# Performance work log

Measured on AMD Instinct MI355X. Metric: run time of the kernel, lower is better.

The kernel has to match this reference:

```python
import jax, jax.numpy as jnp
import numpy as np
import math

B, S, E = 4, 2048, 1024


def setup_inputs() -> dict:
    key = jax.random.key(0)
    ks = jax.random.split(key, 7)
    w_scale = 1.0 / math.sqrt(E)
    x = jax.random.normal(ks[0], (B, S, E), dtype=jnp.float32)
    Wq = jax.random.normal(ks[1], (E, E), dtype=jnp.float32) * w_scale
    bq = jax.random.normal(ks[2], (E,), dtype=jnp.float32) * 0.01
    Wk = jax.random.normal(ks[3], (E, E), dtype=jnp.float32) * w_scale
    bk = jax.random.normal(ks[4], (E,), dtype=jnp.float32) * 0.01
    Wv = jax.random.normal(ks[5], (E, E), dtype=jnp.float32) * w_scale
    bv = jax.random.normal(ks[6], (E,), dtype=jnp.float32) * 0.01
    # causal mask: True = attend, False = masked (mask == 0 -> -inf)
    mask = jnp.broadcast_to(jnp.tril(jnp.ones((S, S), dtype=bool)), (B, S, S))
    return {"x": x, "Wq": Wq, "bq": bq, "Wk": Wk, "bk": bk, "Wv": Wv, "bv": bv, "mask": mask}


def reference(x, Wq, bq, Wk, bk, Wv, bv, mask):
    # nn.Linear stores weight as [out, in]: y = x @ W.T + b
    Q = jnp.einsum("bse,oe->bso", x, Wq) + bq
    K = jnp.einsum("bse,oe->bso", x, Wk) + bk
    V = jnp.einsum("bse,oe->bso", x, Wv) + bv
    scale = math.sqrt(E)
    scores = jnp.einsum("bqe,bke->bqk", Q, K) / scale  # [B,S,S]
    scores = jnp.where(mask, scores, -jnp.inf)
    attn = jax.nn.softmax(scores, axis=-1)
    out = jnp.einsum("bqk,bke->bqe", attn, V)  # [B,S,E]
    return out
```

## Files before the change

kernel.cpp:

```cpp
#include <hip/hip_runtime.h>
#include <stdint.h>

typedef unsigned short u16;
typedef __attribute__((ext_vector_type(8))) short bf16x8;
typedef __attribute__((ext_vector_type(4))) float f32x4;

#define MFMA16(a, b, c) __builtin_amdgcn_mfma_f32_16x16x32_bf16((a), (b), (c), 0, 0, 0)

#define MASKVAL (-1.0e30f)

__device__ __forceinline__ u16 f2bf(float f) {
  union { float f; uint32_t u; } v; v.f = f;
  uint32_t u = v.u;
  u += 0x7fffu + ((u >> 16) & 1u);
  return (u16)(u >> 16);
}
__device__ __forceinline__ void async16(const void* g, void* l) {
  __builtin_amdgcn_global_load_lds(
      (const __attribute__((address_space(1))) unsigned int*)g,
      (__attribute__((address_space(3))) unsigned int*)l, 16, 0, 0);
}

__global__ __launch_bounds__(256) void conv_kernel(
    const float* __restrict__ x,  const float* __restrict__ wq,
    const float* __restrict__ wk, const float* __restrict__ wv,
    u16* __restrict__ xb, u16* __restrict__ wb, int do_wv)
{
  const int NX = 1 << 20;
  const int NW = 1 << 17;
  const int total = NX + NW * (do_wv ? 3 : 2);
  for (int i = blockIdx.x * 256 + threadIdx.x; i < total; i += gridDim.x * 256) {
    const float* src; u16* dst;
    if (i < NX) {
      src = x + (size_t)i * 8;
      const int m = i >> 7, k8 = i & 127;
      dst = xb + (size_t)m * 2048 + 1024 + k8 * 8;
    } else {
      const int j = i - NX;
      const int wsel = j >> 17;
      const int jj = j & (NW - 1);
      const float* W = (wsel == 0) ? wq : (wsel == 1) ? wk : wv;
      const int zoff = (wsel == 0) ? 0 : (wsel == 1) ? (2 << 20) : (1 << 20);
      src = W + (size_t)jj * 8;
      dst = wb + zoff + jj * 8;
    }
    float4 f0 = *(const float4*)src;
    float4 f1 = *(const float4*)(src + 4);
    ushort4 h0, h1;
    h0.x = f2bf(f0.x); h0.y = f2bf(f0.y); h0.z = f2bf(f0.z); h0.w = f2bf(f0.w);
    h1.x = f2bf(f1.x); h1.y = f2bf(f1.y); h1.z = f2bf(f1.z); h1.w = f2bf(f1.w);
    *(ushort4*)dst = h0;
    *(ushort4*)(dst + 4) = h1;
  }
}

template <int BMODE>
__global__ __launch_bounds__(256) void gemm_kernel(
    const u16* __restrict__ xb,
    const u16* __restrict__ wb,
    const float* __restrict__ wv_f,
    const float* __restrict__ bq, const float* __restrict__ bk,
    const float* __restrict__ bv,
    u16* __restrict__ q_out, u16* __restrict__ vt_out, u16* __restrict__ k_out,
    int zbase, int zmul)
{
  const int z = zbase + (int)blockIdx.z * zmul;
  __shared__ u16 lA[2][128 * 32];
  __shared__ u16 lB[2][128 * 32];

  const int m0 = blockIdx.x * 128, n0 = blockIdx.y * 128;
  const int tid = threadIdx.x, lane = tid & 63, w = tid >> 6;
  const int quad = lane >> 4, l15 = lane & 15;
  const int wr = (w >> 1) * 64, wc = (w & 1) * 64;

  const u16* wz = wb + ((size_t)z << 20);
  const float* bias = (z == 0) ? bq : (z == 1) ? bv : bk;

  const int sr  = lane >> 2;
  const int ssw = (lane >> 3) & 3;
  const int c16s = (lane & 3) ^ ssw;

  auto stageA = [&](int kk, int bbuf) {
    const int k0 = kk * 32;
#pragma unroll
    for (int i = 0; i < 2; ++i) {
      const int r = w * 32 + i * 16 + sr;
      async16(&xb[(size_t)(m0 + r) * 2048 + 1024 + k0 + c16s * 8],
              &lA[bbuf][w * 1024 + i * 512]);
    }
  };
  auto stageB = [&](int kk, int bbuf) {
    const int k0 = kk * 32;
#pragma unroll
    for (int i = 0; i < 2; ++i) {
      const int r = w * 32 + i * 16 + sr;
      async16(&wz[(size_t)(n0 + r) * 1024 + k0 + c16s * 8],
              &lB[bbuf][w * 1024 + i * 512]);
    }
  };

  float4 bfr[4];
  const int br = tid >> 1;
  const int bcb = (tid & 1) * 2;
  const int bs = (br >> 1) & 3;
  auto loadB = [&](int kk) {
    const float* p = &wv_f[(size_t)(n0 + br) * 1024 + kk * 32 + bcb * 8];
    bfr[0] = ((const float4*)p)[0];
    bfr[1] = ((const float4*)p)[1];
    bfr[2] = ((const float4*)p)[2];
    bfr[3] = ((const float4*)p)[3];
  };
  auto writeB = [&](int bbuf) {
    ushort4 h[4];
#pragma unroll
    for (int g = 0; g < 4; ++g) {
      h[g].x = f2bf(bfr[g].x); h[g].y = f2bf(bfr[g].y);
      h[g].z = f2bf(bfr[g].z); h[g].w = f2bf(bfr[g].w);
    }
    const int p0 = (bcb + 0) ^ bs, p1 = (bcb + 1) ^ bs;
    *(ushort4*)&lB[bbuf][br * 32 + p0 * 8]     = h[0];
    *(ushort4*)&lB[bbuf][br * 32 + p0 * 8 + 4] = h[1];
    *(ushort4*)&lB[bbuf][br * 32 + p1 * 8]     = h[2];
    *(ushort4*)&lB[bbuf][br * 32 + p1 * 8 + 4] = h[3];
  };

  f32x4 zero4 = {0.f, 0.f, 0.f, 0.f};
  f32x4 acc[4][4];
#pragma unroll
  for (int i = 0; i < 4; ++i)
#pragma unroll
    for (int j = 0; j < 4; ++j) acc[i][j] = zero4;

  if constexpr (BMODE == 0) {
    stageA(0, 0); stageB(0, 0);
  } else {
    stageA(0, 0); loadB(0); writeB(0);
  }

  const int fxor = (l15 >> 1) & 3;
  for (int kk = 0; kk < 32; ++kk) {
    const int bbuf = kk & 1;
    __syncthreads();
    if (kk + 1 < 32) {
      stageA(kk + 1, bbuf ^ 1);
      if constexpr (BMODE == 0) stageB(kk + 1, bbuf ^ 1);
      else loadB(kk + 1);
    }
    bf16x8 af[4], bw[4];
#pragma unroll
    for (int mf = 0; mf < 4; ++mf)
      af[mf] = *(const bf16x8*)
          &lA[bbuf][(wr + mf * 16 + l15) * 32 + (quad ^ fxor) * 8];
#pragma unroll
    for (int nf = 0; nf < 4; ++nf)
      bw[nf] = *(const bf16x8*)
          &lB[bbuf][(wc + nf * 16 + l15) * 32 + (quad ^ fxor) * 8];
#pragma unroll
    for (int mf = 0; mf < 4; ++mf)
#pragma unroll
      for (int nf = 0; nf < 4; ++nf)
        acc[mf][nf] = MFMA16(af[mf], bw[nf], acc[mf][nf]);
    if constexpr (BMODE == 1) {
      if (kk + 1 < 32) writeB(bbuf ^ 1);
    }
  }

  float bvv[4];
#pragma unroll
  for (int nf = 0; nf < 4; ++nf)
    bvv[nf] = bias[n0 + wc + nf * 16 + l15];

  if (z == 0) {
    const float qs = 0.03125f;
#pragma unroll
    for (int mf = 0; mf < 4; ++mf) {
#pragma unroll
      for (int nf = 0; nf < 4; ++nf) {
        const int n = n0 + wc + nf * 16 + l15;
#pragma unroll
        for (int r = 0; r < 4; ++r) {
          const int m = m0 + wr + mf * 16 + quad * 4 + r;
          q_out[(size_t)m * 2048 + n] = f2bf((acc[mf][nf][r] + bvv[nf]) * qs);
        }
      }
    }
  } else if (z == 1) {
#pragma unroll
    for (int mf = 0; mf < 4; ++mf) {
      const int mbase = m0 + wr + mf * 16 + quad * 4;
      const int bb = mbase >> 11;
      const int ss = mbase & 2047;
#pragma unroll
      for (int nf = 0; nf < 4; ++nf) {
        const int n = n0 + wc + nf * 16 + l15;
        ushort4 pk;
        pk.x = f2bf(acc[mf][nf][0] + bvv[nf]);
        pk.y = f2bf(acc[mf][nf][1] + bvv[nf]);
        pk.z = f2bf(acc[mf][nf][2] + bvv[nf]);
        pk.w = f2bf(acc[mf][nf][3] + bvv[nf]);
        *(ushort4*)&vt_out[((size_t)bb << 21) + (size_t)n * 2048 + ss] = pk;
      }
    }
  } else {
#pragma unroll
    for (int mf = 0; mf < 4; ++mf) {
#pragma unroll
      for (int nf = 0; nf < 4; ++nf) {
        const int n = n0 + wc + nf * 16 + l15;
#pragma unroll
        for (int r = 0; r < 4; ++r) {
          const int m = m0 + wr + mf * 16 + quad * 4 + r;
          k_out[(size_t)m * 1024 + n] = f2bf(acc[mf][nf][r] + bvv[nf]);
        }
      }
    }
  }
}

__global__ __launch_bounds__(256) void attn_kernel(
    const u16* Q, const u16* __restrict__ K,
    const u16* __restrict__ VT, float* out)
{
  __shared__ u16   sQ[32 * 1024];
  __shared__ u16   sKV[2][128 * 128];
  __shared__ float sS[32 * 132];
  __shared__ u16   sP[32 * 136];
  __shared__ float sAlpha[32];
  __shared__ float sLinv[32];

  const int lin = blockIdx.x + ((int)blockIdx.y << 6);
  const int xcd = lin & 7;
  const int t = ((lin >> 3) << 1) | (xcd & 1);
  const int b = xcd >> 1;
  const int q0 = t * 32;
  const int tid = threadIdx.x, lane = tid & 63, w = tid >> 6;
  const int quad = lane >> 4, l15 = lane & 15;
  const u16* Qb  = Q  + ((size_t)b << 22);
  const u16* Kb  = K  + ((size_t)b << 21);
  const u16* VTb = VT + ((size_t)b << 21);
  float* outb = out + ((size_t)b << 21);

  const int sr = lane >> 4;
  const int sp = lane & 15;

#pragma unroll
  for (int jj = 0; jj < 16; ++jj) {
    const int j = w * 16 + jj;
    const int r = j >> 1;
    const int p = (j & 1) * 64 + lane;
    const int cq = p ^ (r & 15);
    async16(&Qb[(size_t)(q0 + r) * 2048 + (size_t)cq * 8], &sQ[j * 512]);
  }

  auto issueK = [&](int kv0, int e0, u16* buf) {
#pragma unroll
    for (int jj = 0; jj < 8; ++jj) {
      const int j = w * 8 + jj;
      const int r = j * 4 + sr;
      const int c16 = sp ^ (r & 15);
      async16(&Kb[(size_t)(kv0 + r) * 1024 + e0 + c16 * 8], buf + j * 512);
    }
  };
  auto issueV = [&](int kv0, int ck, u16* buf) {
#pragma unroll
    for (int jj = 0; jj < 8; ++jj) {
      const int j = w * 8 + jj;
      const int r = j * 4 + sr;
      const int c16 = sp ^ (r & 15);
      async16(&VTb[(size_t)(ck * 128 + r) * 2048 + kv0 + c16 * 8], buf + j * 512);
    }
  };

  f32x4 zero4 = {0.f, 0.f, 0.f, 0.f};
  f32x4 accO[8][2][2];
#pragma unroll
  for (int c = 0; c < 8; ++c)
#pragma unroll
    for (int i = 0; i < 2; ++i)
#pragma unroll
      for (int j = 0; j < 2; ++j) accO[c][i][j] = zero4;

  float m_i = MASKVAL, l_i = 0.f;
  const int srow = tid >> 3, slane = tid & 7;

  issueK(0, 0, sKV[0]);

  const int niter = q0 / 128 + 1;
  for (int it = 0; it < niter; ++it) {
    const int kv0 = it * 128;

    f32x4 accS[2][2];
#pragma unroll
    for (int i = 0; i < 2; ++i)
#pragma unroll
      for (int j = 0; j < 2; ++j) accS[i][j] = zero4;

#pragma unroll
    for (int c = 0; c < 8; ++c) {
      __syncthreads();
      if (c < 7) issueK(kv0, (c + 1) * 128, sKV[(c + 1) & 1]);
      else       issueV(kv0, 0, sKV[0]);
      const u16* buf = sKV[c & 1];
#pragma unroll
      for (int ks = 0; ks < 4; ++ks) {
        const int cq = c * 16 + ks * 4 + quad;
        const int ck = ks * 4 + quad;
        bf16x8 a0 = *(const bf16x8*)&sQ[l15 * 1024 + (cq ^ l15) * 8];
        bf16x8 a1 = *(const bf16x8*)&sQ[(16 + l15) * 1024 + (cq ^ l15) * 8];
        bf16x8 b0 = *(const bf16x8*)&buf[(w * 32 + l15) * 128 + (ck ^ l15) * 8];
        bf16x8 b1 = *(const bf16x8*)&buf[(w * 32 + 16 + l15) * 128 + (ck ^ l15) * 8];
        accS[0][0] = MFMA16(a0, b0, accS[0][0]);
        accS[0][1] = MFMA16(a0, b1, accS[0][1]);
        accS[1][0] = MFMA16(a1, b0, accS[1][0]);
        accS[1][1] = MFMA16(a1, b1, accS[1][1]);
      }
    }

#pragma unroll
    for (int mf = 0; mf < 2; ++mf)
#pragma unroll
      for (int nf = 0; nf < 2; ++nf)
#pragma unroll
        for (int r = 0; r < 4; ++r) {
          const int row = mf * 16 + quad * 4 + r;
          const int col = w * 32 + nf * 16 + l15;
          sS[row * 132 + col] =
              (kv0 + col <= q0 + row) ? accS[mf][nf][r] : MASKVAL;
        }
    __syncthreads();

    {
      float v[16];
      float4 t0 = *(const float4*)&sS[srow * 132 + slane * 16 + 0];
      float4 t1 = *(const float4*)&sS[srow * 132 + slane * 16 + 4];
      float4 t2 = *(const float4*)&sS[srow * 132 + slane * 16 + 8];
      float4 t3 = *(const float4*)&sS[srow * 132 + slane * 16 + 12];
      v[0]=t0.x; v[1]=t0.y; v[2]=t0.z; v[3]=t0.w;
      v[4]=t1.x; v[5]=t1.y; v[6]=t1.z; v[7]=t1.w;
      v[8]=t2.x; v[9]=t2.y; v[10]=t2.z; v[11]=t2.w;
      v[12]=t3.x; v[13]=t3.y; v[14]=t3.z; v[15]=t3.w;
      float mx = v[0];
#pragma unroll
      for (int j = 1; j < 16; ++j) mx = fmaxf(mx, v[j]);
#pragma unroll
      for (int d = 1; d < 8; d <<= 1) mx = fmaxf(mx, __shfl_xor(mx, d, 64));
      const float mnew  = fmaxf(m_i, mx);
      const float alpha = __expf(m_i - mnew);
      float sum = 0.f;
      u16 pb[16];
#pragma unroll
      for (int j = 0; j < 16; ++j) {
        const float p = __expf(v[j] - mnew);
        pb[j] = f2bf(p);
        union { uint32_t u; float f; } pv; pv.u = ((uint32_t)pb[j]) << 16;
        sum += pv.f;
      }
#pragma unroll
      for (int g = 0; g < 4; ++g) {
        ushort4 pk; pk.x = pb[g*4]; pk.y = pb[g*4+1]; pk.z = pb[g*4+2]; pk.w = pb[g*4+3];
        *(ushort4*)&sP[srow * 136 + slane * 16 + g * 4] = pk;
      }
#pragma unroll
      for (int d = 1; d < 8; d <<= 1) sum += __shfl_xor(sum, d, 64);
      l_i = l_i * alpha + sum;
      m_i = mnew;
      if (slane == 0) sAlpha[srow] = alpha;
      if (it == niter - 1 && slane == 0) sLinv[srow] = 1.0f / l_i;
    }
    __syncthreads();

    float av[2][4];
#pragma unroll
    for (int mf = 0; mf < 2; ++mf)
#pragma unroll
      for (int r = 0; r < 4; ++r)
        av[mf][r] = sAlpha[mf * 16 + quad * 4 + r];
#pragma unroll
    for (int c = 0; c < 8; ++c)
#pragma unroll
      for (int mf = 0; mf < 2; ++mf)
#pragma unroll
        for (int nf = 0; nf < 2; ++nf)
#pragma unroll
          for (int r = 0; r < 4; ++r) accO[c][mf][nf][r] *= av[mf][r];

#pragma unroll
    for (int k = 0; k < 8; ++k) {
      if (k > 0) __syncthreads();
      if (k < 7) issueV(kv0, k + 1, sKV[(k + 1) & 1]);
      else if (it + 1 < niter) issueK(kv0 + 128, 0, sKV[0]);
      const u16* buf = sKV[k & 1];
#pragma unroll
      for (int ks = 0; ks < 4; ++ks) {
        const int ck = ks * 4 + quad;
        bf16x8 p0 = *(const bf16x8*)&sP[l15 * 136 + ks * 32 + quad * 8];
        bf16x8 p1 = *(const bf16x8*)&sP[(16 + l15) * 136 + ks * 32 + quad * 8];
        bf16x8 v0 = *(const bf16x8*)&buf[(w * 32 + l15) * 128 + (ck ^ l15) * 8];
        bf16x8 v1 = *(const bf16x8*)&buf[(w * 32 + 16 + l15) * 128 + (ck ^ l15) * 8];
        accO[k][0][0] = MFMA16(p0, v0, accO[k][0][0]);
        accO[k][0][1] = MFMA16(p0, v1, accO[k][0][1]);
        accO[k][1][0] = MFMA16(p1, v0, accO[k][1][0]);
        accO[k][1][1] = MFMA16(p1, v1, accO[k][1][1]);
      }
    }
  }

  float lv[2][4];
#pragma unroll
  for (int mf = 0; mf < 2; ++mf)
#pragma unroll
    for (int r = 0; r < 4; ++r)
      lv[mf][r] = sLinv[mf * 16 + quad * 4 + r];
#pragma unroll
  for (int c = 0; c < 8; ++c)
#pragma unroll
    for (int mf = 0; mf < 2; ++mf)
#pragma unroll
      for (int nf = 0; nf < 2; ++nf) {
        const int col = c * 128 + w * 32 + nf * 16 + l15;
#pragma unroll
        for (int r = 0; r < 4; ++r) {
          const int row = q0 + mf * 16 + quad * 4 + r;
          outb[(size_t)row * 1024 + col] = accO[c][mf][nf][r] * lv[mf][r];
        }
      }
}

extern "C" void kernel_launch(void* const* d_in, const int* in_sizes, int n_in,
                              void* d_out, int out_size, void* d_ws, size_t ws_size,
                              hipStream_t stream) {
  (void)in_sizes; (void)n_in; (void)out_size;
  const float* x  = (const float*)d_in[0];
  const float* Wq = (const float*)d_in[1];
  const float* bq = (const float*)d_in[2];
  const float* Wk = (const float*)d_in[3];
  const float* bk = (const float*)d_in[4];
  const float* Wv = (const float*)d_in[5];
  const float* bv = (const float*)d_in[6];

  u16* qbuf = (u16*)d_out;
  u16* vtw  = (u16*)d_in[7];
  u16* kw   = (u16*)d_ws;

  const bool ws_big = ws_size >= (size_t)22 * 1024 * 1024;
  u16* wb = ws_big ? (u16*)d_ws + (8u << 20) : (u16*)d_in[7];

  conv_kernel<<<dim3(2048), 256, 0, stream>>>(x, Wq, Wk, Wv, qbuf, wb,
                                              ws_big ? 1 : 0);
  if (ws_big) {
    gemm_kernel<0><<<dim3(64, 8, 3), 256, 0, stream>>>(
        qbuf, wb, Wv, bq, bk, bv, qbuf, vtw, kw, 0, 1);
  } else {
    gemm_kernel<0><<<dim3(64, 8, 2), 256, 0, stream>>>(
        qbuf, wb, Wv, bq, bk, bv, qbuf, vtw, kw, 0, 2);
    gemm_kernel<1><<<dim3(64, 8, 1), 256, 0, stream>>>(
        qbuf, wb, Wv, bq, bk, bv, qbuf, vtw, kw, 1, 1);
  }

  attn_kernel<<<dim3(64, 4), 256, 0, stream>>>(qbuf, kw, vtw, (float*)d_out);
}
```

Measured before the change: 435.0 us.

## Restructure attention kernel to 512 threads with triple-buffered K/V/Q ring

The attention kernel now runs 8 waves per block instead of 4, each wave owning 16 key/value columns, and the whole-Q shared tile is replaced by streaming Q chunks alongside K chunks. A three-slot ring buffer with explicit vmcnt waits and raw barriers replaces double buffering with __syncthreads, so loads are issued two stages ahead. This is meant to raise latency hiding and reduce LDS footprint and per-thread accumulator registers. It adds redundant Q reloads every kv iteration and depends on hand-tuned waitcnt values being correct.

New measurement: 414.4 us. -4.7%, faster.

```diff
diff --git a/kernel.cpp b/kernel.cpp
--- a/kernel.cpp
+++ b/kernel.cpp
@@ -8,6 +8,10 @@
 #define MFMA16(a, b, c) __builtin_amdgcn_mfma_f32_16x16x32_bf16((a), (b), (c), 0, 0, 0)
 
 #define MASKVAL (-1.0e30f)
+
+#define WAITV(N) asm volatile("s_waitcnt vmcnt(" #N ")" ::: "memory")
+#define LGKM0()  asm volatile("s_waitcnt lgkmcnt(0)" ::: "memory")
+#define SBAR()   __builtin_amdgcn_s_barrier()
 
 __device__ __forceinline__ u16 f2bf(float f) {
   union { float f; uint32_t u; } v; v.f = f;
@@ -217,12 +221,12 @@
   }
 }
 
-__global__ __launch_bounds__(256) void attn_kernel(
-    const u16* Q, const u16* __restrict__ K,
+__global__ __launch_bounds__(512) void attn_kernel(
+    const u16* __restrict__ Q, const u16* __restrict__ K,
     const u16* __restrict__ VT, float* out)
 {
-  __shared__ u16   sQ[32 * 1024];
-  __shared__ u16   sKV[2][128 * 128];
+  constexpr int SLOT = 20480;
+  __shared__ u16   ring[3][SLOT];
   __shared__ float sS[32 * 132];
   __shared__ u16   sP[32 * 136];
   __shared__ float sAlpha[32];
@@ -243,131 +247,122 @@
   const int sr = lane >> 4;
   const int sp = lane & 15;
 
-#pragma unroll
-  for (int jj = 0; jj < 16; ++jj) {
-    const int j = w * 16 + jj;
-    const int r = j >> 1;
-    const int p = (j & 1) * 64 + lane;
-    const int cq = p ^ (r & 15);
-    async16(&Qb[(size_t)(q0 + r) * 2048 + (size_t)cq * 8], &sQ[j * 512]);
-  }
-
-  auto issueK = [&](int kv0, int e0, u16* buf) {
-#pragma unroll
-    for (int jj = 0; jj < 8; ++jj) {
-      const int j = w * 8 + jj;
+  auto issueK = [&](int kv0, int e0, u16* slot) {
+#pragma unroll
+    for (int jj = 0; jj < 4; ++jj) {
+      const int j = w * 4 + jj;
       const int r = j * 4 + sr;
       const int c16 = sp ^ (r & 15);
-      async16(&Kb[(size_t)(kv0 + r) * 1024 + e0 + c16 * 8], buf + j * 512);
-    }
-  };
-  auto issueV = [&](int kv0, int ck, u16* buf) {
-#pragma unroll
-    for (int jj = 0; jj < 8; ++jj) {
-      const int j = w * 8 + jj;
+      async16(&Kb[(size_t)(kv0 + r) * 1024 + e0 + c16 * 8], slot + j * 512);
+    }
+  };
+  auto issueV = [&](int kv0, int ck, u16* slot) {
+#pragma unroll
+    for (int jj = 0; jj < 4; ++jj) {
+      const int j = w * 4 + jj;
       const int r = j * 4 + sr;
       const int c16 = sp ^ (r & 15);
-      async16(&VTb[(size_t)(ck * 128 + r) * 2048 + kv0 + c16 * 8], buf + j * 512);
-    }
+      async16(&VTb[(size_t)(ck * 128 + r) * 2048 + kv0 + c16 * 8], slot + j * 512);
+    }
+  };
+  auto issueQ = [&](int cq, u16* slot) {
+    const int r = w * 4 + sr;
+    const int c16 = sp ^ (r & 15);
+    async16(&Qb[(size_t)(q0 + r) * 2048 + cq * 128 + c16 * 8],
+            slot + 16384 + w * 512);
   };
 
   f32x4 zero4 = {0.f, 0.f, 0.f, 0.f};
-  f32x4 accO[8][2][2];
+  f32x4 accO[8][2];
 #pragma unroll
   for (int c = 0; c < 8; ++c)
 #pragma unroll
-    for (int i = 0; i < 2; ++i)
-#pragma unroll
-      for (int j = 0; j < 2; ++j) accO[c][i][j] = zero4;
+    for (int i = 0; i < 2; ++i) accO[c][i] = zero4;
 
   float m_i = MASKVAL, l_i = 0.f;
-  const int srow = tid >> 3, slane = tid & 7;
-
-  issueK(0, 0, sKV[0]);
+  const int srow = tid >> 4, slane = tid & 15;
+
+  issueK(0, 0, ring[0]);   issueQ(0, ring[0]);
+  issueK(0, 128, ring[1]); issueQ(1, ring[1]);
+  int sl = 0, sl2 = 2;
 
   const int niter = q0 / 128 + 1;
   for (int it = 0; it < niter; ++it) {
     const int kv0 = it * 128;
 
-    f32x4 accS[2][2];
-#pragma unroll
-    for (int i = 0; i < 2; ++i)
-#pragma unroll
-      for (int j = 0; j < 2; ++j) accS[i][j] = zero4;
+    f32x4 accS[2];
+    accS[0] = zero4; accS[1] = zero4;
 
 #pragma unroll
     for (int c = 0; c < 8; ++c) {
-      __syncthreads();
-      if (c < 7) issueK(kv0, (c + 1) * 128, sKV[(c + 1) & 1]);
-      else       issueV(kv0, 0, sKV[0]);
-      const u16* buf = sKV[c & 1];
+      if (c < 7) { WAITV(5); } else { WAITV(4); }
+      SBAR();
+      u16* dst = ring[sl2];
+      if (c < 6)      { issueK(kv0, (c + 2) * 128, dst); issueQ(c + 2, dst); }
+      else if (c == 6) issueV(kv0, 0, dst);
+      else             issueV(kv0, 1, dst);
+      const u16* bufK = ring[sl];
+      const u16* bufQ = ring[sl] + 16384;
 #pragma unroll
       for (int ks = 0; ks < 4; ++ks) {
-        const int cq = c * 16 + ks * 4 + quad;
-        const int ck = ks * 4 + quad;
-        bf16x8 a0 = *(const bf16x8*)&sQ[l15 * 1024 + (cq ^ l15) * 8];
-        bf16x8 a1 = *(const bf16x8*)&sQ[(16 + l15) * 1024 + (cq ^ l15) * 8];
-        bf16x8 b0 = *(const bf16x8*)&buf[(w * 32 + l15) * 128 + (ck ^ l15) * 8];
-        bf16x8 b1 = *(const bf16x8*)&buf[(w * 32 + 16 + l15) * 128 + (ck ^ l15) * 8];
-        accS[0][0] = MFMA16(a0, b0, accS[0][0]);
-        accS[0][1] = MFMA16(a0, b1, accS[0][1]);
-        accS[1][0] = MFMA16(a1, b0, accS[1][0]);
-        accS[1][1] = MFMA16(a1, b1, accS[1][1]);
-      }
+        const int cc = ks * 4 + quad;
+        bf16x8 a0 = *(const bf16x8*)&bufQ[l15 * 128 + (cc ^ l15) * 8];
+        bf16x8 a1 = *(const bf16x8*)&bufQ[(16 + l15) * 128 + (cc ^ l15) * 8];
+        bf16x8 b0 = *(const bf16x8*)&bufK[(w * 16 + l15) * 128 + (cc ^ l15) * 8];
+        accS[0] = MFMA16(a0, b0, accS[0]);
+        accS[1] = MFMA16(a1, b0, accS[1]);
+      }
+      sl  = (sl  == 2) ? 0 : sl  + 1;
+      sl2 = (sl2 == 2) ? 0 : sl2 + 1;
     }
 
 #pragma unroll
     for (int mf = 0; mf < 2; ++mf)
 #pragma unroll
-      for (int nf = 0; nf < 2; ++nf)
-#pragma unroll
-        for (int r = 0; r < 4; ++r) {
-          const int row = mf * 16 + quad * 4 + r;
-          const int col = w * 32 + nf * 16 + l15;
-          sS[row * 132 + col] =
-              (kv0 + col <= q0 + row) ? accS[mf][nf][r] : MASKVAL;
-        }
-    __syncthreads();
+      for (int r = 0; r < 4; ++r) {
+        const int row = mf * 16 + quad * 4 + r;
+        const int col = w * 16 + l15;
+        sS[row * 132 + col] = (kv0 + col <= q0 + row) ? accS[mf][r] : MASKVAL;
+      }
+    LGKM0();
+    SBAR();
 
     {
-      float v[16];
-      float4 t0 = *(const float4*)&sS[srow * 132 + slane * 16 + 0];
-      float4 t1 = *(const float4*)&sS[srow * 132 + slane * 16 + 4];
-      float4 t2 = *(const float4*)&sS[srow * 132 + slane * 16 + 8];
-      float4 t3 = *(const float4*)&sS[srow * 132 + slane * 16 + 12];
+      float v[8];
+      float4 t0 = *(const float4*)&sS[srow * 132 + slane * 8 + 0];
+      float4 t1 = *(const float4*)&sS[srow * 132 + slane * 8 + 4];
       v[0]=t0.x; v[1]=t0.y; v[2]=t0.z; v[3]=t0.w;
       v[4]=t1.x; v[5]=t1.y; v[6]=t1.z; v[7]=t1.w;
-      v[8]=t2.x; v[9]=t2.y; v[10]=t2.z; v[11]=t2.w;
-      v[12]=t3.x; v[13]=t3.y; v[14]=t3.z; v[15]=t3.w;
       float mx = v[0];
 #pragma unroll
-      for (int j = 1; j < 16; ++j) mx = fmaxf(mx, v[j]);
-#pragma unroll
-      for (int d = 1; d < 8; d <<= 1) mx = fmaxf(mx, __shfl_xor(mx, d, 64));
+      for (int j = 1; j < 8; ++j) mx = fmaxf(mx, v[j]);
+#pragma unroll
+      for (int d = 1; d < 16; d <<= 1) mx = fmaxf(mx, __shfl_xor(mx, d, 64));
       const float mnew  = fmaxf(m_i, mx);
       const float alpha = __expf(m_i - mnew);
       float sum = 0.f;
-      u16 pb[16];
-#pragma unroll
-      for (int j = 0; j < 16; ++j) {
+      u16 pb[8];
+#pragma unroll
+      for (int j = 0; j < 8; ++j) {
         const float p = __expf(v[j] - mnew);
         pb[j] = f2bf(p);
         union { uint32_t u; float f; } pv; pv.u = ((uint32_t)pb[j]) << 16;
         sum += pv.f;
       }
-#pragma unroll
-      for (int g = 0; g < 4; ++g) {
-        ushort4 pk; pk.x = pb[g*4]; pk.y = pb[g*4+1]; pk.z = pb[g*4+2]; pk.w = pb[g*4+3];
-        *(ushort4*)&sP[srow * 136 + slane * 16 + g * 4] = pk;
-      }
-#pragma unroll
-      for (int d = 1; d < 8; d <<= 1) sum += __shfl_xor(sum, d, 64);
+      ushort4 pk0, pk1;
+      pk0.x = pb[0]; pk0.y = pb[1]; pk0.z = pb[2]; pk0.w = pb[3];
+      pk1.x = pb[4]; pk1.y = pb[5]; pk1.z = pb[6]; pk1.w = pb[7];
+      *(ushort4*)&sP[srow * 136 + slane * 8 + 0] = pk0;
+      *(ushort4*)&sP[srow * 136 + slane * 8 + 4] = pk1;
+#pragma unroll
+      for (int d = 1; d < 16; d <<= 1) sum += __shfl_xor(sum, d, 64);
       l_i = l_i * alpha + sum;
       m_i = mnew;
       if (slane == 0) sAlpha[srow] = alpha;
       if (it == niter - 1 && slane == 0) sLinv[srow] = 1.0f / l_i;
     }
-    __syncthreads();
+    LGKM0();
+    SBAR();
 
     float av[2][4];
 #pragma unroll
@@ -380,28 +375,32 @@
 #pragma unroll
       for (int mf = 0; mf < 2; ++mf)
 #pragma unroll
-        for (int nf = 0; nf < 2; ++nf)
-#pragma unroll
-          for (int r = 0; r < 4; ++r) accO[c][mf][nf][r] *= av[mf][r];
+        for (int r = 0; r < 4; ++r) accO[c][mf][r] *= av[mf][r];
 
 #pragma unroll
     for (int k = 0; k < 8; ++k) {
-      if (k > 0) __syncthreads();
-      if (k < 7) issueV(kv0, k + 1, sKV[(k + 1) & 1]);
-      else if (it + 1 < niter) issueK(kv0 + 128, 0, sKV[0]);
-      const u16* buf = sKV[k & 1];
+      if (k < 7)                 { WAITV(4); }
+      else if (it + 1 < niter)   { WAITV(5); }
+      else                       { WAITV(0); }
+      SBAR();
+      u16* dst = ring[sl2];
+      if (k < 6) issueV(kv0, k + 2, dst);
+      else if (it + 1 < niter) {
+        issueK(kv0 + 128, (k - 6) * 128, dst);
+        issueQ(k - 6, dst);
+      }
+      const u16* bufV = ring[sl];
 #pragma unroll
       for (int ks = 0; ks < 4; ++ks) {
-        const int ck = ks * 4 + quad;
-        bf16x8 p0 = *(const bf16x8*)&sP[l15 * 136 + ks * 32 + quad * 8];
-        bf16x8 p1 = *(const bf16x8*)&sP[(16 + l15) * 136 + ks * 32 + quad * 8];
-        bf16x8 v0 = *(const bf16x8*)&buf[(w * 32 + l15) * 128 + (ck ^ l15) * 8];
-        bf16x8 v1 = *(const bf16x8*)&buf[(w * 32 + 16 + l15) * 128 + (ck ^ l15) * 8];
-        accO[k][0][0] = MFMA16(p0, v0, accO[k][0][0]);
-        accO[k][0][1] = MFMA16(p0, v1, accO[k][0][1]);
-        accO[k][1][0] = MFMA16(p1, v0, accO[k][1][0]);
-        accO[k][1][1] = MFMA16(p1, v1, accO[k][1][1]);
-      }
+        const int cc = ks * 4 + quad;
+        bf16x8 p0 = *(const bf16x8*)&sP[l15 * 136 + cc * 8];
+        bf16x8 p1 = *(const bf16x8*)&sP[(16 + l15) * 136 + cc * 8];
+        bf16x8 v0 = *(const bf16x8*)&bufV[(w * 16 + l15) * 128 + (cc ^ l15) * 8];
+        accO[k][0] = MFMA16(p0, v0, accO[k][0]);
+        accO[k][1] = MFMA16(p1, v0, accO[k][1]);
+      }
+      sl  = (sl  == 2) ? 0 : sl  + 1;
+      sl2 = (sl2 == 2) ? 0 : sl2 + 1;
     }
   }
 
@@ -414,16 +413,14 @@
 #pragma unroll
   for (int c = 0; c < 8; ++c)
 #pragma unroll
-    for (int mf = 0; mf < 2; ++mf)
-#pragma unroll
-      for (int nf = 0; nf < 2; ++nf) {
-        const int col = c * 128 + w * 32 + nf * 16 + l15;
-#pragma unroll
-        for (int r = 0; r < 4; ++r) {
-          const int row = q0 + mf * 16 + quad * 4 + r;
-          outb[(size_t)row * 1024 + col] = accO[c][mf][nf][r] * lv[mf][r];
-        }
-      }
+    for (int mf = 0; mf < 2; ++mf) {
+      const int col = c * 128 + w * 16 + l15;
+#pragma unroll
+      for (int r = 0; r < 4; ++r) {
+        const int row = q0 + mf * 16 + quad * 4 + r;
+        outb[(size_t)row * 1024 + col] = accO[c][mf][r] * lv[mf][r];
+      }
+    }
 }
 
 extern "C" void kernel_launch(void* const* d_in, const int* in_sizes, int n_in,
@@ -457,5 +454,5 @@
         qbuf, wb, Wv, bq, bk, bv, qbuf, vtw, kw, 1, 1);
   }
 
-  attn_kernel<<<dim3(64, 4), 256, 0, stream>>>(qbuf, kw, vtw, (float*)d_out);
-}
+  attn_kernel<<<dim3(64, 4), 512, 0, stream>>>(qbuf, kw, vtw, (float*)d_out);
+}
```
